# Kernel optimization log

Hardware: AMD Instinct MI355X
Metric: run time of the kernel (lower is better)

Reference implementation:

```python
import jax, jax.numpy as jnp
import numpy as np

N, C, S = 2, 512, 256
SCALE = 2.0

def setup_inputs() -> dict:
    key = jax.random.key(0)
    kq, kk, kv = jax.random.split(key, 3)
    q = jax.random.normal(kq, (N, C, S), dtype=jnp.float32)
    k = jax.random.normal(kk, (N, C, S), dtype=jnp.float32)
    v = jax.random.normal(kv, (N, C, S), dtype=jnp.float32)
    return {"q": q, "k": k, "v": v}

def reference(q, k, v):
    # q: (N,C,S) -> (N,C,1,S); k: (N,C,S) -> (N,1,C,S)
    # weights[n,c,d] = -sum_s |k[n,d,s] - q[n,c,s]| / scale
    diff = jnp.abs(k[:, None, :, :] - q[:, :, None, :])  # (N,C,C,S)
    weights = -(diff / SCALE).sum(axis=-1)               # (N,C,C)
    weights = jax.nn.softmax(weights, axis=-1)
    rep = jnp.einsum('ncd,nds->ncs', weights, v)         # (N,C,S)
    return rep
```

## Files before the change

### kernel.cpp

```cpp
#include <hip/hip_runtime.h>
#include <hip/hip_bf16.h>


constexpr int N_ = 2;
constexpr int C_ = 512;
constexpr int S_ = 256;
constexpr int TC = 4;
constexpr int NW = 4;

template <int CTRL, int ROW_MASK>
__device__ __forceinline__ float dpp_add(float x) {
    int yi = __builtin_amdgcn_update_dpp(0, __float_as_int(x), CTRL, ROW_MASK, 0xf, true);
    return x + __int_as_float(yi);
}
template <int CTRL, int ROW_MASK>
__device__ __forceinline__ float dpp_max(float x) {
    int yi = __builtin_amdgcn_update_dpp(__float_as_int(x), __float_as_int(x), CTRL, ROW_MASK, 0xf, false);
    return fmaxf(x, __int_as_float(yi));
}
__device__ __forceinline__ float dpp_reduce_halves(float x) {
    x = dpp_add<0x111, 0xf>(x);
    x = dpp_add<0x112, 0xf>(x);
    x = dpp_add<0x114, 0xf>(x);
    x = dpp_add<0x118, 0xf>(x);
    x = dpp_add<0x142, 0xa>(x);
    return x;
}
__device__ __forceinline__ float wave_sum_bcast(float x) {
    x = dpp_reduce_halves(x);
    x = dpp_add<0x143, 0xc>(x);
    return __int_as_float(__builtin_amdgcn_readlane(__float_as_int(x), 63));
}
__device__ __forceinline__ float wave_max_bcast(float x) {
    x = dpp_max<0x111, 0xf>(x);
    x = dpp_max<0x112, 0xf>(x);
    x = dpp_max<0x114, 0xf>(x);
    x = dpp_max<0x118, 0xf>(x);
    x = dpp_max<0x142, 0xa>(x);
    x = dpp_max<0x143, 0xc>(x);
    return __int_as_float(__builtin_amdgcn_readlane(__float_as_int(x), 63));
}

template <int DSPLIT>
__global__ __launch_bounds__(256, 4)
void laplace_attn_main(const float* __restrict__ q,
                       const float* __restrict__ k,
                       const float* __restrict__ v,
                       float* __restrict__ ws) {
    constexpr int DH  = C_ / DSPLIT;
    constexpr int DPW = DH / NW;
    constexpr int E   = DH / 64;
    constexpr size_t PO_SZ = (size_t)N_ * C_ * DSPLIT * S_;
    constexpr size_t ST_SZ = (size_t)N_ * C_ * DSPLIT;

    const int b      = blockIdx.x;
    constexpr int per_n = (C_ / TC) * DSPLIT;
    const int n    = b / per_n;
    const int r    = b - n * per_n;
    const int half = r % DSPLIT;
    const int c0   = (r / DSPLIT) * TC;
    const int tid  = threadIdx.x;
    const int w    = tid >> 6;
    const int lane = tid & 63;

    const float* kbase = k + (size_t)n * C_ * S_;
    const float* vbase = v + (size_t)n * C_ * S_;

    float* po = ws;
    float* pm = ws + PO_SZ;
    float* pl = pm + ST_SZ;

    __shared__ float4 wt[DH];
    __shared__ float4 accs[NW][TC][64];

    const int h = lane >> 5;
    const int j = lane & 31;
    float4 qa[TC], qb[TC];
    #pragma unroll
    for (int c = 0; c < TC; ++c) {
        const float4* qr = (const float4*)(q + ((size_t)n * C_ + c0 + c) * S_);
        qa[c] = qr[2 * j];
        qb[c] = qr[2 * j + 1];
    }

    const int dw0 = half * DH + w * DPW;
    const float* kw = kbase + (size_t)dw0 * S_;

    #pragma unroll 2
    for (int g2 = 0; g2 < DPW; g2 += 2) {
        const float4* rp = (const float4*)(kw + (size_t)(g2 + h) * S_ + j * 8);
        const float4 ka = rp[0];
        const float4 kb = rp[1];
        float s0[TC], s1[TC];
        #pragma unroll
        for (int c = 0; c < TC; ++c) {
            float p = fabsf(ka.x - qa[c].x) + fabsf(ka.y - qa[c].y)
                    + fabsf(ka.z - qa[c].z) + fabsf(ka.w - qa[c].w)
                    + fabsf(kb.x - qb[c].x) + fabsf(kb.y - qb[c].y)
                    + fabsf(kb.z - qb[c].z) + fabsf(kb.w - qb[c].w);
            p = dpp_reduce_halves(p);
            s0[c] = __int_as_float(__builtin_amdgcn_readlane(__float_as_int(p), 31));
            s1[c] = __int_as_float(__builtin_amdgcn_readlane(__float_as_int(p), 63));
        }
        if (lane == 0) {
            wt[w * DPW + g2]     = make_float4(-0.5f * s0[0], -0.5f * s0[1],
                                               -0.5f * s0[2], -0.5f * s0[3]);
            wt[w * DPW + g2 + 1] = make_float4(-0.5f * s1[0], -0.5f * s1[1],
                                               -0.5f * s1[2], -0.5f * s1[3]);
        }
    }
    __syncthreads();

    {
        const float* wtf = (const float*)wt;
        float x[E];
        #pragma unroll
        for (int e = 0; e < E; ++e) x[e] = wtf[(lane + 64 * e) * 4 + w];
        float m = x[0];
        #pragma unroll
        for (int e = 1; e < E; ++e) m = fmaxf(m, x[e]);
        m = wave_max_bcast(m);
        float es[E], l = 0.f;
        #pragma unroll
        for (int e = 0; e < E; ++e) { es[e] = __expf(x[e] - m); l += es[e]; }
        l = wave_sum_bcast(l);
        float* wtm = (float*)wt;
        #pragma unroll
        for (int e = 0; e < E; ++e) wtm[(lane + 64 * e) * 4 + w] = es[e];
        if (lane == 0) {
            const size_t sidx = ((size_t)n * C_ + c0 + w) * DSPLIT + half;
            pm[sidx] = m;
            pl[sidx] = l;
        }
    }
    __syncthreads();

    float4 acc[TC];
    #pragma unroll
    for (int c = 0; c < TC; ++c) acc[c] = make_float4(0.f, 0.f, 0.f, 0.f);

    const float4* v4 = (const float4*)(vbase + (size_t)dw0 * S_);
    #pragma unroll 4
    for (int dd = 0; dd < DPW; ++dd) {
        const float4 vv = v4[dd * 64 + lane];
        const float4 ww = wt[w * DPW + dd];
        acc[0].x += ww.x * vv.x; acc[0].y += ww.x * vv.y;
        acc[0].z += ww.x * vv.z; acc[0].w += ww.x * vv.w;
        acc[1].x += ww.y * vv.x; acc[1].y += ww.y * vv.y;
        acc[1].z += ww.y * vv.z; acc[1].w += ww.y * vv.w;
        acc[2].x += ww.z * vv.x; acc[2].y += ww.z * vv.y;
        acc[2].z += ww.z * vv.z; acc[2].w += ww.z * vv.w;
        acc[3].x += ww.w * vv.x; acc[3].y += ww.w * vv.y;
        acc[3].z += ww.w * vv.z; acc[3].w += ww.w * vv.w;
    }
    #pragma unroll
    for (int c = 0; c < TC; ++c) accs[w][c][lane] = acc[c];
    __syncthreads();

    {
        const int c = w;
        float4 a  = accs[0][c][lane];
        float4 bq = accs[1][c][lane];
        float4 cc = accs[2][c][lane];
        float4 dq = accs[3][c][lane];
        float4 o;
        o.x = (a.x + bq.x) + (cc.x + dq.x);
        o.y = (a.y + bq.y) + (cc.y + dq.y);
        o.z = (a.z + bq.z) + (cc.z + dq.z);
        o.w = (a.w + bq.w) + (cc.w + dq.w);
        const size_t oidx = (((size_t)n * C_ + c0 + c) * DSPLIT + half) * S_;
        ((float4*)(po + oidx))[lane] = o;
    }
}

template <int DSPLIT>
__global__ __launch_bounds__(64)
void laplace_attn_combine(const float* __restrict__ ws,
                          float* __restrict__ out) {
    constexpr size_t PO_SZ = (size_t)N_ * C_ * DSPLIT * S_;
    constexpr size_t ST_SZ = (size_t)N_ * C_ * DSPLIT;
    const int b    = blockIdx.x;
    const int lane = threadIdx.x;

    const float* po = ws;
    const float* pm = ws + PO_SZ;
    const float* pl = pm + ST_SZ;

    float m[DSPLIT], l[DSPLIT];
    #pragma unroll
    for (int hh = 0; hh < DSPLIT; ++hh) {
        m[hh] = pm[(size_t)b * DSPLIT + hh];
        l[hh] = pl[(size_t)b * DSPLIT + hh];
    }
    float M = m[0];
    #pragma unroll
    for (int hh = 1; hh < DSPLIT; ++hh) M = fmaxf(M, m[hh]);
    float den = 0.f, a[DSPLIT];
    #pragma unroll
    for (int hh = 0; hh < DSPLIT; ++hh) { a[hh] = __expf(m[hh] - M); den += a[hh] * l[hh]; }
    const float inv = 1.f / den;

    float4 rsum = make_float4(0.f, 0.f, 0.f, 0.f);
    #pragma unroll
    for (int hh = 0; hh < DSPLIT; ++hh) {
        const float4 o = ((const float4*)(po + ((size_t)b * DSPLIT + hh) * S_))[lane];
        rsum.x += a[hh] * o.x;
        rsum.y += a[hh] * o.y;
        rsum.z += a[hh] * o.z;
        rsum.w += a[hh] * o.w;
    }
    float4 rr;
    rr.x = rsum.x * inv; rr.y = rsum.y * inv;
    rr.z = rsum.z * inv; rr.w = rsum.w * inv;
    ((float4*)(out + (size_t)b * S_))[lane] = rr;
}

extern "C" void kernel_launch(void* const* d_in, const int* in_sizes, int n_in,
                              void* d_out, int out_size, void* d_ws, size_t ws_size,
                              hipStream_t stream) {
    const float* q = (const float*)d_in[0];
    const float* k = (const float*)d_in[1];
    const float* v = (const float*)d_in[2];
    float* out = (float*)d_out;
    float* ws  = (float*)d_ws;

    constexpr size_t NEED4 =
        ((size_t)N_ * C_ * 4 * S_ + 2 * (size_t)N_ * C_ * 4) * sizeof(float);

    if (ws_size >= NEED4) {
        laplace_attn_main<4><<<dim3(N_ * (C_ / TC) * 4), dim3(256), 0, stream>>>(q, k, v, ws);
        laplace_attn_combine<4><<<dim3(N_ * C_), dim3(64), 0, stream>>>(ws, out);
    } else {
        laplace_attn_main<2><<<dim3(N_ * (C_ / TC) * 2), dim3(256), 0, stream>>>(q, k, v, ws);
        laplace_attn_combine<2><<<dim3(N_ * C_), dim3(64), 0, stream>>>(ws, out);
    }
}
```

Baseline: 77.76 us.

## Tile L1 distance with shared-memory K chunks and per-thread 2x2 register blocking

Replaces the per-pair cross-lane DPP reduction in the distance phase with a register-blocked scheme. Q rows and chunks of K are staged in LDS, the next K chunk is prefetched through registers, and each thread accumulates partial sums for 2 query rows by several key rows, so no cross-lane reduction is needed. Query rows per block double to 8, which halves the number of blocks and doubles how often each V load is reused. The cost is more LDS, more registers (occupancy hint lowered from 4 to 2) and extra barriers per chunk.

```diff
diff --git a/kernel.cpp b/kernel.cpp
--- a/kernel.cpp
+++ b/kernel.cpp
@@ -1,11 +1,10 @@
 #include <hip/hip_runtime.h>
-#include <hip/hip_bf16.h>
 
 
 constexpr int N_ = 2;
 constexpr int C_ = 512;
 constexpr int S_ = 256;
-constexpr int TC = 4;
+constexpr int TC = 8;
 constexpr int NW = 4;
 
 template <int CTRL, int ROW_MASK>
@@ -18,16 +17,12 @@
     int yi = __builtin_amdgcn_update_dpp(__float_as_int(x), __float_as_int(x), CTRL, ROW_MASK, 0xf, false);
     return fmaxf(x, __int_as_float(yi));
 }
-__device__ __forceinline__ float dpp_reduce_halves(float x) {
+__device__ __forceinline__ float wave_sum_bcast(float x) {
     x = dpp_add<0x111, 0xf>(x);
     x = dpp_add<0x112, 0xf>(x);
     x = dpp_add<0x114, 0xf>(x);
     x = dpp_add<0x118, 0xf>(x);
     x = dpp_add<0x142, 0xa>(x);
-    return x;
-}
-__device__ __forceinline__ float wave_sum_bcast(float x) {
-    x = dpp_reduce_halves(x);
     x = dpp_add<0x143, 0xc>(x);
     return __int_as_float(__builtin_amdgcn_readlane(__float_as_int(x), 63));
 }
@@ -42,18 +37,37 @@
 }
 
 template <int DSPLIT>
-__global__ __launch_bounds__(256, 4)
-void laplace_attn_main(const float* __restrict__ q,
-                       const float* __restrict__ k,
-                       const float* __restrict__ v,
+__global__ __launch_bounds__(256, 2)
+void laplace_attn_main(const float* __restrict__ qg,
+                       const float* __restrict__ kg,
+                       const float* __restrict__ vg,
                        float* __restrict__ ws) {
-    constexpr int DH  = C_ / DSPLIT;
-    constexpr int DPW = DH / NW;
-    constexpr int E   = DH / 64;
+    constexpr int DH   = C_ / DSPLIT;
+    constexpr int DPW  = DH / NW;
+    constexpr int DSUB = DPW / 32;
+    constexpr int SC   = (DSPLIT >= 4) ? 64 : 32;
+    constexpr int SC4  = SC / 4;
+    constexpr int NCH  = S_ / SC;
+    constexpr int KST  = SC + 4;
+    constexpr int QST  = S_ + 4;
+    constexpr int E    = DH / 64;
+    constexpr int KF4  = DH * SC4 / 256;
     constexpr size_t PO_SZ = (size_t)N_ * C_ * DSPLIT * S_;
     constexpr size_t ST_SZ = (size_t)N_ * C_ * DSPLIT;
 
-    const int b      = blockIdx.x;
+    constexpr int QS_BYTES = TC * QST * 4;
+    constexpr int WT_BYTES = DH * TC * 4;
+    constexpr int KS_BYTES = DH * KST * 4;
+    constexpr int AC_BYTES = NW * TC * (S_ / 4) * 16;
+    constexpr int U_BYTES  = (KS_BYTES > AC_BYTES) ? KS_BYTES : AC_BYTES;
+
+    __shared__ __align__(16) char smem_raw[QS_BYTES + WT_BYTES + U_BYTES];
+    float  (*qs)[QST]        = (float (*)[QST])smem_raw;
+    float  (*wtT)[TC]        = (float (*)[TC])(smem_raw + QS_BYTES);
+    float  (*ksm)[KST]       = (float (*)[KST])(smem_raw + QS_BYTES + WT_BYTES);
+    float4 (*accs)[TC][S_/4] = (float4 (*)[TC][S_/4])(smem_raw + QS_BYTES + WT_BYTES);
+
+    const int b = blockIdx.x;
     constexpr int per_n = (C_ / TC) * DSPLIT;
     const int n    = b / per_n;
     const int r    = b - n * per_n;
@@ -62,114 +76,168 @@
     const int tid  = threadIdx.x;
     const int w    = tid >> 6;
     const int lane = tid & 63;
-
-    const float* kbase = k + (size_t)n * C_ * S_;
-    const float* vbase = v + (size_t)n * C_ * S_;
+    const int cg   = lane >> 4;
+    const int dg   = lane & 15;
 
     float* po = ws;
     float* pm = ws + PO_SZ;
     float* pl = pm + ST_SZ;
 
-    __shared__ float4 wt[DH];
-    __shared__ float4 accs[NW][TC][64];
-
-    const int h = lane >> 5;
-    const int j = lane & 31;
-    float4 qa[TC], qb[TC];
-    #pragma unroll
-    for (int c = 0; c < TC; ++c) {
-        const float4* qr = (const float4*)(q + ((size_t)n * C_ + c0 + c) * S_);
-        qa[c] = qr[2 * j];
-        qb[c] = qr[2 * j + 1];
-    }
-
-    const int dw0 = half * DH + w * DPW;
-    const float* kw = kbase + (size_t)dw0 * S_;
-
-    #pragma unroll 2
-    for (int g2 = 0; g2 < DPW; g2 += 2) {
-        const float4* rp = (const float4*)(kw + (size_t)(g2 + h) * S_ + j * 8);
-        const float4 ka = rp[0];
-        const float4 kb = rp[1];
-        float s0[TC], s1[TC];
-        #pragma unroll
-        for (int c = 0; c < TC; ++c) {
-            float p = fabsf(ka.x - qa[c].x) + fabsf(ka.y - qa[c].y)
-                    + fabsf(ka.z - qa[c].z) + fabsf(ka.w - qa[c].w)
-                    + fabsf(kb.x - qb[c].x) + fabsf(kb.y - qb[c].y)
-                    + fabsf(kb.z - qb[c].z) + fabsf(kb.w - qb[c].w);
-            p = dpp_reduce_halves(p);
-            s0[c] = __int_as_float(__builtin_amdgcn_readlane(__float_as_int(p), 31));
-            s1[c] = __int_as_float(__builtin_amdgcn_readlane(__float_as_int(p), 63));
-        }
-        if (lane == 0) {
-            wt[w * DPW + g2]     = make_float4(-0.5f * s0[0], -0.5f * s0[1],
-                                               -0.5f * s0[2], -0.5f * s0[3]);
-            wt[w * DPW + g2 + 1] = make_float4(-0.5f * s1[0], -0.5f * s1[1],
-                                               -0.5f * s1[2], -0.5f * s1[3]);
-        }
+    {
+        const float* qrow = qg + ((size_t)n * C_ + c0) * S_;
+        #pragma unroll
+        for (int it = 0; it < 2; ++it) {
+            const int f   = tid + 256 * it;
+            const int row = f >> 6;
+            const int col = (f & 63) << 2;
+            const float4 val = *(const float4*)(qrow + (size_t)row * S_ + col);
+            *(float4*)&qs[row][col] = val;
+        }
+    }
+
+    const float* krow0 = kg + ((size_t)n * C_ + half * DH) * S_;
+
+    float4 kreg[KF4];
+    #pragma unroll
+    for (int it = 0; it < KF4; ++it) {
+        const int f   = tid + 256 * it;
+        const int row = f / SC4;
+        const int col = (f % SC4) << 2;
+        kreg[it] = *(const float4*)(krow0 + (size_t)row * S_ + col);
+    }
+    #pragma unroll
+    for (int it = 0; it < KF4; ++it) {
+        const int f   = tid + 256 * it;
+        const int row = f / SC4;
+        const int col = (f % SC4) << 2;
+        *(float4*)&ksm[row][col] = kreg[it];
     }
     __syncthreads();
 
-    {
-        const float* wtf = (const float*)wt;
+    float acc[2][DSUB][2];
+    #pragma unroll
+    for (int i = 0; i < 2; ++i)
+        #pragma unroll
+        for (int sub = 0; sub < DSUB; ++sub)
+            #pragma unroll
+            for (int j = 0; j < 2; ++j) acc[i][sub][j] = 0.f;
+
+    for (int ch = 0; ch < NCH; ++ch) {
+        if (ch + 1 < NCH) {
+            const float* kc = krow0 + (ch + 1) * SC;
+            #pragma unroll
+            for (int it = 0; it < KF4; ++it) {
+                const int f   = tid + 256 * it;
+                const int row = f / SC4;
+                const int col = (f % SC4) << 2;
+                kreg[it] = *(const float4*)(kc + (size_t)row * S_ + col);
+            }
+        }
+        const int sbase = ch * SC;
+        #pragma unroll
+        for (int t = 0; t < SC4; ++t) {
+            const int sl = t << 2;
+            const int sq = sbase + sl;
+            float4 qf0 = *(const float4*)&qs[2 * cg + 0][sq];
+            float4 qf1 = *(const float4*)&qs[2 * cg + 1][sq];
+            #pragma unroll
+            for (int sub = 0; sub < DSUB; ++sub) {
+                #pragma unroll
+                for (int j = 0; j < 2; ++j) {
+                    const int dl = w * DPW + sub * 32 + dg + 16 * j;
+                    const float4 kf = *(const float4*)&ksm[dl][sl];
+                    acc[0][sub][j] += (fabsf(kf.x - qf0.x) + fabsf(kf.y - qf0.y))
+                                    + (fabsf(kf.z - qf0.z) + fabsf(kf.w - qf0.w));
+                    acc[1][sub][j] += (fabsf(kf.x - qf1.x) + fabsf(kf.y - qf1.y))
+                                    + (fabsf(kf.z - qf1.z) + fabsf(kf.w - qf1.w));
+                }
+            }
+        }
+        __syncthreads();
+        if (ch + 1 < NCH) {
+            #pragma unroll
+            for (int it = 0; it < KF4; ++it) {
+                const int f   = tid + 256 * it;
+                const int row = f / SC4;
+                const int col = (f % SC4) << 2;
+                *(float4*)&ksm[row][col] = kreg[it];
+            }
+            __syncthreads();
+        }
+    }
+
+    #pragma unroll
+    for (int sub = 0; sub < DSUB; ++sub)
+        #pragma unroll
+        for (int j = 0; j < 2; ++j) {
+            const int dl = w * DPW + sub * 32 + dg + 16 * j;
+            wtT[dl][2 * cg + 0] = -0.5f * acc[0][sub][j];
+            wtT[dl][2 * cg + 1] = -0.5f * acc[1][sub][j];
+        }
+    __syncthreads();
+
+    #pragma unroll
+    for (int cc = 0; cc < 2; ++cc) {
+        const int c = 2 * w + cc;
         float x[E];
         #pragma unroll
-        for (int e = 0; e < E; ++e) x[e] = wtf[(lane + 64 * e) * 4 + w];
+        for (int e = 0; e < E; ++e) x[e] = wtT[lane + 64 * e][c];
         float m = x[0];
         #pragma unroll
         for (int e = 1; e < E; ++e) m = fmaxf(m, x[e]);
         m = wave_max_bcast(m);
-        float es[E], l = 0.f;
-        #pragma unroll
-        for (int e = 0; e < E; ++e) { es[e] = __expf(x[e] - m); l += es[e]; }
+        float l = 0.f;
+        #pragma unroll
+        for (int e = 0; e < E; ++e) { x[e] = __expf(x[e] - m); l += x[e]; }
         l = wave_sum_bcast(l);
-        float* wtm = (float*)wt;
-        #pragma unroll
-        for (int e = 0; e < E; ++e) wtm[(lane + 64 * e) * 4 + w] = es[e];
+        #pragma unroll
+        for (int e = 0; e < E; ++e) wtT[lane + 64 * e][c] = x[e];
         if (lane == 0) {
-            const size_t sidx = ((size_t)n * C_ + c0 + w) * DSPLIT + half;
+            const size_t sidx = ((size_t)n * C_ + c0 + c) * DSPLIT + half;
             pm[sidx] = m;
             pl[sidx] = l;
         }
     }
     __syncthreads();
 
-    float4 acc[TC];
-    #pragma unroll
-    for (int c = 0; c < TC; ++c) acc[c] = make_float4(0.f, 0.f, 0.f, 0.f);
-
-    const float4* v4 = (const float4*)(vbase + (size_t)dw0 * S_);
+    float4 oa[TC];
+    #pragma unroll
+    for (int c = 0; c < TC; ++c) oa[c] = make_float4(0.f, 0.f, 0.f, 0.f);
+
+    const float4* v4 = (const float4*)(vg + ((size_t)n * C_ + half * DH) * S_);
     #pragma unroll 4
     for (int dd = 0; dd < DPW; ++dd) {
-        const float4 vv = v4[dd * 64 + lane];
-        const float4 ww = wt[w * DPW + dd];
-        acc[0].x += ww.x * vv.x; acc[0].y += ww.x * vv.y;
-        acc[0].z += ww.x * vv.z; acc[0].w += ww.x * vv.w;
-        acc[1].x += ww.y * vv.x; acc[1].y += ww.y * vv.y;
-        acc[1].z += ww.y * vv.z; acc[1].w += ww.y * vv.w;
-        acc[2].x += ww.z * vv.x; acc[2].y += ww.z * vv.y;
-        acc[2].z += ww.z * vv.z; acc[2].w += ww.z * vv.w;
-        acc[3].x += ww.w * vv.x; acc[3].y += ww.w * vv.y;
-        acc[3].z += ww.w * vv.z; acc[3].w += ww.w * vv.w;
-    }
-    #pragma unroll
-    for (int c = 0; c < TC; ++c) accs[w][c][lane] = acc[c];
+        const int dl = w * DPW + dd;
+        const float4 vv = v4[(size_t)dl * (S_ / 4) + lane];
+        const float4 w0 = *(const float4*)&wtT[dl][0];
+        const float4 w1 = *(const float4*)&wtT[dl][4];
+        const float wc[TC] = {w0.x, w0.y, w0.z, w0.w, w1.x, w1.y, w1.z, w1.w};
+        #pragma unroll
+        for (int c = 0; c < TC; ++c) {
+            oa[c].x += wc[c] * vv.x; oa[c].y += wc[c] * vv.y;
+            oa[c].z += wc[c] * vv.z; oa[c].w += wc[c] * vv.w;
+        }
+    }
+    #pragma unroll
+    for (int c = 0; c < TC; ++c) accs[w][c][lane] = oa[c];
     __syncthreads();
 
-    {
-        const int c = w;
-        float4 a  = accs[0][c][lane];
-        float4 bq = accs[1][c][lane];
-        float4 cc = accs[2][c][lane];
-        float4 dq = accs[3][c][lane];
+    #pragma unroll
+    for (int it = 0; it < 2; ++it) {
+        const int slot = tid + 256 * it;
+        const int c  = slot >> 6;
+        const int ln = slot & 63;
+        const float4 a0 = accs[0][c][ln];
+        const float4 a1 = accs[1][c][ln];
+        const float4 a2 = accs[2][c][ln];
+        const float4 a3 = accs[3][c][ln];
         float4 o;
-        o.x = (a.x + bq.x) + (cc.x + dq.x);
-        o.y = (a.y + bq.y) + (cc.y + dq.y);
-        o.z = (a.z + bq.z) + (cc.z + dq.z);
-        o.w = (a.w + bq.w) + (cc.w + dq.w);
+        o.x = (a0.x + a1.x) + (a2.x + a3.x);
+        o.y = (a0.y + a1.y) + (a2.y + a3.y);
+        o.z = (a0.z + a1.z) + (a2.z + a3.z);
+        o.w = (a0.w + a1.w) + (a2.w + a3.w);
         const size_t oidx = (((size_t)n * C_ + c0 + c) * DSPLIT + half) * S_;
-        ((float4*)(po + oidx))[lane] = o;
+        ((float4*)(po + oidx))[ln] = o;
     }
 }
 
```

Result: slower. 170.5 us (+119.3%).
